# Kernel tuning notes

Hardware: AMD Instinct MI355X
Metric: run time of the kernel (lower is better)

The kernel has to match this reference:

```python
import jax, jax.numpy as jnp
import numpy as np

CHANNELS = 256
REDUCTION = 4
REDUCED = max(1, CHANNELS // REDUCTION)  # 64


def setup_inputs() -> dict:
    key = jax.random.key(0)
    kx, kq, kk, kv, ko = jax.random.split(key, 5)
    B, C, H, W = 4, CHANNELS, 48, 48
    x = jax.random.normal(kx, (B, C, H, W), dtype=jnp.float32)
    # 1x1 conv weights (bias=False) for 3 q/k/v branches, stored as [3, reduced, C]
    wq = jax.random.normal(kq, (3, REDUCED, C), dtype=jnp.float32) * 0.05
    wk = jax.random.normal(kk, (3, REDUCED, C), dtype=jnp.float32) * 0.05
    wv = jax.random.normal(kv, (3, REDUCED, C), dtype=jnp.float32) * 0.05
    # output 1x1 conv: [C, 3*reduced]
    wo = jax.random.normal(ko, (C, 3 * REDUCED), dtype=jnp.float32) * 0.05
    return {"x": x, "wq": wq, "wk": wk, "wv": wv, "wo": wo}


def reference(x, wq, wk, wv, wo):
    B, C, H, W = x.shape
    N = H * W
    r = wq.shape[1]
    scale = 1.0 / float(r) ** 0.5
    xf = x.reshape(B, C, N)                      # [B, C, N]
    # 1x1 convs == channel matmuls; all 3 branches at once
    qs = jnp.einsum('irc,bcn->ibrn', wq, xf)     # [3, B, r, N]
    ks = jnp.einsum('irc,bcn->ibrn', wk, xf)
    vs = jnp.einsum('irc,bcn->ibrn', wv, xf)
    outs = []
    for i in range(3):                           # structural 3x3 nesting
        q = qs[i]                                # [B, r, N]
        acc = jnp.zeros((B, r, N), dtype=x.dtype)
        for j in range(3):
            # attn[b, n, m] = softmax_m(q[b,:,n] . k[b,:,m] / sqrt(r))
            attn = jax.nn.softmax(jnp.einsum('brn,brm->bnm', q, ks[j]) * scale, axis=-1)
            acc = acc + jnp.einsum('brm,bnm->brn', vs[j], attn)
        outs.append(acc)
    combined = jnp.concatenate(outs, axis=1)     # [B, 3r, N]
    out = jnp.einsum('cr,brn->bcn', wo, combined).reshape(B, C, H, W)
    return x * jax.nn.sigmoid(out)
```

## Files before the change

kernel.cpp:

```cpp
#include <hip/hip_runtime.h>


#define BB 4
#define CC 256
#define NN_ 2304
#define RR 64

#define OQ 0
#define OK_ 1769472
#define OV 3538944
#define OC 5308416
#define CSTR 1769472
#define FR_IB 147456
#define OXF 10616832
#define OWF 12976128
#define OWOF 13123584

typedef __bf16 bf16x8 __attribute__((ext_vector_type(8)));
typedef float f32x16 __attribute__((ext_vector_type(16)));
typedef unsigned short ushort8 __attribute__((ext_vector_type(8)));
typedef unsigned int uintx2 __attribute__((ext_vector_type(2)));
typedef unsigned int uintx4 __attribute__((ext_vector_type(4)));

#if __has_builtin(__builtin_amdgcn_exp2f)
#define EXP2(x) __builtin_amdgcn_exp2f(x)
#else
#define EXP2(x) exp2f(x)
#endif

__device__ __forceinline__ float bf2f(unsigned short s) {
    unsigned int u = ((unsigned int)s) << 16;
    return __builtin_bit_cast(float, u);
}
__device__ __forceinline__ unsigned int pk_bf16(float lo, float hi) {
    unsigned int r;
    asm("v_cvt_pk_bf16_f32 %0, %1, %2" : "=v"(r) : "v"(lo), "v"(hi));
    return r;
}

__global__ __launch_bounds__(256) void prep_kernel(
    const float* __restrict__ x, const float* __restrict__ wq,
    const float* __restrict__ wk, const float* __restrict__ wv,
    const float* __restrict__ wo, unsigned short* __restrict__ wsb)
{
    int bid = blockIdx.x;
    int t = threadIdx.x;
    if (bid < 9) {
        int s = bid;
        int type = s / 3, i = s % 3;
        const float* wsel = (type == 0) ? wq : (type == 1 ? wk : wv);
        const float scale = (type == 0) ? 0.18033688011112042f : 1.0f;
        unsigned short* dst = wsb + OWF + s * 16384;
        #pragma unroll
        for (int p = 0; p < 8; ++p) {
            int u = t + 256 * p;
            int ks = u >> 7, rb = (u >> 6) & 1, lo = u & 63;
            int row = rb * 32 + (lo & 31), c = ks * 16 + 8 * (lo >> 5);
            const float* src = wsel + ((i * 64 + row) * 256 + c);
            float4 f0 = *(const float4*)(src);
            float4 f1 = *(const float4*)(src + 4);
            uintx4 pwv = {pk_bf16(f0.x * scale, f0.y * scale),
                          pk_bf16(f0.z * scale, f0.w * scale),
                          pk_bf16(f1.x * scale, f1.y * scale),
                          pk_bf16(f1.z * scale, f1.w * scale)};
            *(uintx4*)(dst + (ks * 2 + rb) * 512 + lo * 8) = pwv;
        }
        return;
    }
    if (bid < 12) {
        int bb = bid - 9;
        #pragma unroll
        for (int p = 0; p < 8; ++p) {
            int u = t + 256 * p;
            int cg = bb * 32 + (u >> 6);
            int lane = u & 63;
            int ks = cg >> 3, rb = cg & 7;
            int row = rb * 32 + (lane & 31);
            int g = ks * 16 + 8 * (lane >> 5);
            const float* src = wo + row * 192 + g;
            float4 f0 = *(const float4*)(src);
            float4 f1 = *(const float4*)(src + 4);
            uintx4 pwv = {pk_bf16(f0.x, f0.y), pk_bf16(f0.z, f0.w),
                          pk_bf16(f1.x, f1.y), pk_bf16(f1.z, f1.w)};
            *(uintx4*)(wsb + OWOF + cg * 512 + lane * 8) = pwv;
        }
        return;
    }
    __shared__ __align__(16) float xs[64 * 132];
    int xb = bid - 12;
    int cq  = xb & 3;
    int nt2 = (xb >> 2) % 18;
    int b   = xb / 72;
    int c0 = cq * 64, n0 = nt2 * 128;
    #pragma unroll
    for (int p = 0; p < 8; ++p) {
        int u = t + 256 * p;
        int cl = u >> 5, nq = (u & 31) * 4;
        *(float4*)&xs[cl * 132 + nq] =
            *(const float4*)&x[((size_t)(b * CC + c0 + cl)) * NN_ + n0 + nq];
    }
    __syncthreads();
    unsigned short* xfb = wsb + OXF + ((size_t)b) * 72 * 16 * 512;
    #pragma unroll
    for (int p = 0; p < 4; ++p) {
        int u = t + 256 * p;
        int nb_l = u >> 8, ks_l = (u >> 6) & 3, lo = u & 63;
        int hh = lo >> 5, idx = lo & 31;
        int clb = ks_l * 16 + 8 * hh;
        int nn = nb_l * 32 + idx;
        unsigned int pw[4];
        #pragma unroll
        for (int d = 0; d < 4; ++d) {
            float a  = xs[(clb + 2 * d) * 132 + nn];
            float bb2 = xs[(clb + 2 * d + 1) * 132 + nn];
            pw[d] = pk_bf16(a, bb2);
        }
        int nb = nt2 * 4 + nb_l, ks = cq * 4 + ks_l;
        *(uintx4*)(xfb + (nb * 16 + ks) * 512 + lo * 8) =
            (uintx4){pw[0], pw[1], pw[2], pw[3]};
    }
}

__global__ __launch_bounds__(256) void proj_mfma(unsigned short* __restrict__ wsb)
{
    int bid = blockIdx.x;
    int s = bid / 72;
    int rem = bid % 72;
    int b = rem / 18, nb4 = rem % 18;
    int type = s / 3, i = s % 3;
    int t = threadIdx.x;
    int w = t >> 6, lane = t & 63;
    int lq = lane & 31, h = lane >> 5;
    int nb = nb4 * 4 + w;

    const unsigned short* wf = wsb + OWF + s * 16384 + lane * 8;
    const unsigned short* xf = wsb + OXF + ((size_t)(b * 72 + nb) * 16) * 512 + lane * 8;

    f32x16 o0 = {}, o1 = {};
    if (type < 2) {
        #pragma unroll
        for (int ks = 0; ks < 16; ++ks) {
            bf16x8 a0 = *(const bf16x8*)(wf + ks * 1024);
            bf16x8 a1 = *(const bf16x8*)(wf + ks * 1024 + 512);
            bf16x8 bx = *(const bf16x8*)(xf + ks * 512);
            o0 = __builtin_amdgcn_mfma_f32_32x32x16_bf16(a0, bx, o0, 0, 0, 0);
            o1 = __builtin_amdgcn_mfma_f32_32x32x16_bf16(a1, bx, o1, 0, 0, 0);
        }
    } else {
        #pragma unroll
        for (int ks = 0; ks < 16; ++ks) {
            bf16x8 a0 = *(const bf16x8*)(wf + ks * 1024);
            bf16x8 a1 = *(const bf16x8*)(wf + ks * 1024 + 512);
            bf16x8 bx = *(const bf16x8*)(xf + ks * 512);
            o0 = __builtin_amdgcn_mfma_f32_32x32x16_bf16(bx, a0, o0, 0, 0, 0);
            o1 = __builtin_amdgcn_mfma_f32_32x32x16_bf16(bx, a1, o1, 0, 0, 0);
        }
    }

    unsigned short* dstbase =
        wsb + ((type == 0) ? OQ : (type == 1 ? OK_ : OV)) +
        ((size_t)(i * 4 + b)) * FR_IB + nb * 2048;

    if (type < 2) {
        #pragma unroll
        for (int g = 0; g < 4; ++g) {
            int kd = 8 * g + 4 * h;
            int off = (kd >> 4) * 512 + ((kd >> 3) & 1) * 256 + lq * 8 + (kd & 7);
            *(uintx2*)(dstbase + off) =
                (uintx2){pk_bf16(o0[4 * g], o0[4 * g + 1]),
                         pk_bf16(o0[4 * g + 2], o0[4 * g + 3])};
            int kd2 = kd + 32;
            int off2 = (kd2 >> 4) * 512 + ((kd2 >> 3) & 1) * 256 + lq * 8 + (kd2 & 7);
            *(uintx2*)(dstbase + off2) =
                (uintx2){pk_bf16(o1[4 * g], o1[4 * g + 1]),
                         pk_bf16(o1[4 * g + 2], o1[4 * g + 3])};
        }
    } else {
        #pragma unroll
        for (int g = 0; g < 4; ++g) {
            int off = (g >> 1) * 1024 + (g & 1) * 256 + lq * 8 + 4 * h;
            *(uintx2*)(dstbase + off) =
                (uintx2){pk_bf16(o0[4 * g], o0[4 * g + 1]),
                         pk_bf16(o0[4 * g + 2], o0[4 * g + 3])};
            *(uintx2*)(dstbase + off + 512) =
                (uintx2){pk_bf16(o1[4 * g], o1[4 * g + 1]),
                         pk_bf16(o1[4 * g + 2], o1[4 * g + 3])};
        }
    }
}

__global__ __launch_bounds__(256, 4) void attn_kernel(unsigned short* __restrict__ wsb)
{
    __shared__ __align__(16) float fl[4352];

    int bid = blockIdx.x;
    int wid = (bid & 7) * 162 + (bid >> 3);
    int s12 = wid / 108;
    int rem = wid % 108;
    int j = s12 >> 2, b = s12 & 3;
    int i = rem / 36;
    int qp = rem % 36;
    int w = threadIdx.x >> 6;
    int ks = w & 1, qloc = w >> 1;
    int lane = threadIdx.x & 63;
    int lq = lane & 31;
    int h = lane >> 5;
    int q0 = (qp * 2 + qloc) * 32;
    int nt = q0 >> 5;

    const unsigned short* qtf = wsb + OQ + ((size_t)(i * 4 + b)) * FR_IB +
                                nt * 2048 + lane * 8;
    const unsigned short* kp = wsb + OK_ + ((size_t)(j * 4 + b)) * FR_IB +
                               (size_t)(ks * 36) * 2048 + lane * 8;
    const unsigned short* vp = wsb + OV + ((size_t)(j * 4 + b)) * FR_IB +
                               (size_t)(ks * 36) * 2048 + lane * 8;

    bf16x8 bq0 = *(const bf16x8*)(qtf + 0);
    bf16x8 bq1 = *(const bf16x8*)(qtf + 512);
    bf16x8 bq2 = *(const bf16x8*)(qtf + 1024);
    bf16x8 bq3 = *(const bf16x8*)(qtf + 1536);

    uintx4 onesw = {0x3F803F80u, 0x3F803F80u, 0x3F803F80u, 0x3F803F80u};
    bf16x8 ones = __builtin_bit_cast(bf16x8, onesw);

    f32x16 o0 = {}, o1 = {}, lacc = {};

    for (int step = 0; step < 36; ++step) {
        const unsigned short* kb = kp + (size_t)step * 2048;
        const unsigned short* vb = vp + (size_t)step * 2048;
        bf16x8 k0 = *(const bf16x8*)(kb + 0 * 512);
        bf16x8 k1 = *(const bf16x8*)(kb + 1 * 512);
        bf16x8 k2 = *(const bf16x8*)(kb + 2 * 512);
        bf16x8 k3 = *(const bf16x8*)(kb + 3 * 512);
        bf16x8 v00 = *(const bf16x8*)(vb + 0 * 512);
        bf16x8 v10 = *(const bf16x8*)(vb + 1 * 512);
        bf16x8 v01 = *(const bf16x8*)(vb + 2 * 512);
        bf16x8 v11 = *(const bf16x8*)(vb + 3 * 512);

        f32x16 s = {};
        __builtin_amdgcn_s_setprio(1);
        s = __builtin_amdgcn_mfma_f32_32x32x16_bf16(k0, bq0, s, 0, 0, 0);
        s = __builtin_amdgcn_mfma_f32_32x32x16_bf16(k1, bq1, s, 0, 0, 0);
        s = __builtin_amdgcn_mfma_f32_32x32x16_bf16(k2, bq2, s, 0, 0, 0);
        s = __builtin_amdgcn_mfma_f32_32x32x16_bf16(k3, bq3, s, 0, 0, 0);
        __builtin_amdgcn_s_setprio(0);

        #pragma unroll
        for (int r = 0; r < 16; ++r) s[r] = EXP2(s[r]);

        __builtin_amdgcn_s_setprio(1);
        {
            unsigned int a0 = pk_bf16(s[0], s[1]);
            unsigned int a1 = pk_bf16(s[2], s[3]);
            unsigned int b0 = pk_bf16(s[4], s[5]);
            unsigned int b1 = pk_bf16(s[6], s[7]);
            uintx2 r0 = __builtin_amdgcn_permlane32_swap(a0, b0, false, false);
            uintx2 r1 = __builtin_amdgcn_permlane32_swap(a1, b1, false, false);
            uintx4 pwv = {r0[0], r1[0], r0[1], r1[1]};
            bf16x8 pa = __builtin_bit_cast(bf16x8, pwv);
            o0 = __builtin_amdgcn_mfma_f32_32x32x16_bf16(v00, pa, o0, 0, 0, 0);
            o1 = __builtin_amdgcn_mfma_f32_32x32x16_bf16(v10, pa, o1, 0, 0, 0);
            lacc = __builtin_amdgcn_mfma_f32_32x32x16_bf16(ones, pa, lacc, 0, 0, 0);
        }
        {
            unsigned int a0 = pk_bf16(s[8], s[9]);
            unsigned int a1 = pk_bf16(s[10], s[11]);
            unsigned int b0 = pk_bf16(s[12], s[13]);
            unsigned int b1 = pk_bf16(s[14], s[15]);
            uintx2 r0 = __builtin_amdgcn_permlane32_swap(a0, b0, false, false);
            uintx2 r1 = __builtin_amdgcn_permlane32_swap(a1, b1, false, false);
            uintx4 pwv = {r0[0], r1[0], r0[1], r1[1]};
            bf16x8 pa = __builtin_bit_cast(bf16x8, pwv);
            o0 = __builtin_amdgcn_mfma_f32_32x32x16_bf16(v01, pa, o0, 0, 0, 0);
            o1 = __builtin_amdgcn_mfma_f32_32x32x16_bf16(v11, pa, o1, 0, 0, 0);
            lacc = __builtin_amdgcn_mfma_f32_32x32x16_bf16(ones, pa, lacc, 0, 0, 0);
        }
        __builtin_amdgcn_s_setprio(0);
    }

    float l_full = lacc[0];

    int off = qloc * 2112;
    if (ks == 1) {
        #pragma unroll
        for (int reg = 0; reg < 16; ++reg) {
            fl[off + reg * 64 + lane] = o0[reg];
            fl[off + 1024 + reg * 64 + lane] = o1[reg];
        }
        fl[off + 2048 + lane] = l_full;
    }
    __syncthreads();
    if (ks == 1) return;

    #pragma unroll
    for (int reg = 0; reg < 16; ++reg) {
        o0[reg] += fl[off + reg * 64 + lane];
        o1[reg] += fl[off + 1024 + reg * 64 + lane];
    }
    float l_tot = l_full + fl[off + 2048 + lane];
    __syncthreads();

    float inv = 1.f / l_tot;
    o0 *= inv; o1 *= inv;

    float* tw = fl + qloc * 2080;
    #pragma unroll
    for (int reg = 0; reg < 16; ++reg) {
        int rv = (reg & 3) + 8 * (reg >> 2) + 4 * h;
        tw[lq * 65 + rv] = o0[reg];
        tw[lq * 65 + 32 + rv] = o1[reg];
    }
    unsigned short* cb = wsb + OC + (size_t)j * CSTR +
                         ((size_t)((b * 72 + nt) * 12 + i * 4)) * 512;
    #pragma unroll
    for (int ksl = 0; ksl < 4; ++ksl) {
        const float* src = tw + lq * 65 + ksl * 16 + 8 * h;
        uintx4 pwv = {pk_bf16(src[0], src[1]), pk_bf16(src[2], src[3]),
                      pk_bf16(src[4], src[5]), pk_bf16(src[6], src[7])};
        *(uintx4*)(cb + ksl * 512 + lane * 8) = pwv;
    }
}

__global__ __launch_bounds__(256) void out_mfma(
    const float* __restrict__ x, const unsigned short* __restrict__ wsb,
    float* __restrict__ out)
{
    int bid = blockIdx.x;
    int ch = bid & 1;
    int nt = (bid >> 1) % 72;
    int b  = bid / 144;
    int n0 = nt * 32;
    int t = threadIdx.x;
    int w = t >> 6, lane = t & 63;
    int lq = lane & 31, h = lane >> 5;
    int rb = ch * 4 + w;

    const unsigned short* wof = wsb + OWOF + lane * 8;
    const unsigned short* cbase = wsb + OC +
        ((size_t)((b * 72 + nt) * 12)) * 512 + lane * 8;

    f32x16 acc = {};
    #pragma unroll
    for (int j = 0; j < 3; ++j) {
        const unsigned short* cj = cbase + (size_t)j * CSTR;
        #pragma unroll
        for (int ksx = 0; ksx < 12; ++ksx) {
            bf16x8 bx = *(const bf16x8*)(cj + ksx * 512);
            bf16x8 a0 = *(const bf16x8*)(wof + (ksx * 8 + rb) * 512);
            acc = __builtin_amdgcn_mfma_f32_32x32x16_bf16(a0, bx, acc, 0, 0, 0);
        }
    }

    int c0 = rb * 32;
    #pragma unroll
    for (int reg = 0; reg < 16; ++reg) {
        int c = c0 + (reg & 3) + 8 * (reg >> 2) + 4 * h;
        size_t idx = ((size_t)(b * CC + c)) * NN_ + n0 + lq;
        float sg = 1.f / (1.f + EXP2(acc[reg] * -1.44269504f));
        out[idx] = x[idx] * sg;
    }
}

extern "C" void kernel_launch(void* const* d_in, const int* in_sizes, int n_in,
                              void* d_out, int out_size, void* d_ws, size_t ws_size,
                              hipStream_t stream) {
    const float* x  = (const float*)d_in[0];
    const float* wq = (const float*)d_in[1];
    const float* wk = (const float*)d_in[2];
    const float* wv = (const float*)d_in[3];
    const float* wo = (const float*)d_in[4];
    unsigned short* wsb = (unsigned short*)d_ws;
    float* out = (float*)d_out;

    prep_kernel<<<300, 256, 0, stream>>>(x, wq, wk, wv, wo, wsb);
    proj_mfma<<<648, 256, 0, stream>>>(wsb);
    attn_kernel<<<1296, 256, 0, stream>>>(wsb);
    out_mfma<<<576, 256, 0, stream>>>(x, wsb, out);
}
```

Before: 102.8 us.

## Prefetch K fragments one step ahead and compute softmax row sums with VALU

The attention inner loop is restructured to double-buffer K fragment loads, issuing the next step's K reads before the current step's MFMAs so global latency overlaps with compute. The per-step ones-vector MFMA used to accumulate the softmax denominator is replaced by scalar float adds of the exponentiated scores, followed by a cross-half-wave shuffle. The s_setprio hints are also removed. These changes cut MFMA work and load stalls, but add register pressure, and the denominator is now summed in fp32 instead of from the bf16-rounded probabilities.

```diff
diff --git a/kernel.cpp b/kernel.cpp
--- a/kernel.cpp
+++ b/kernel.cpp
@@ -220,35 +220,28 @@
     bf16x8 bq2 = *(const bf16x8*)(qtf + 1024);
     bf16x8 bq3 = *(const bf16x8*)(qtf + 1536);
 
-    uintx4 onesw = {0x3F803F80u, 0x3F803F80u, 0x3F803F80u, 0x3F803F80u};
-    bf16x8 ones = __builtin_bit_cast(bf16x8, onesw);
-
-    f32x16 o0 = {}, o1 = {}, lacc = {};
-
-    for (int step = 0; step < 36; ++step) {
-        const unsigned short* kb = kp + (size_t)step * 2048;
+    f32x16 o0 = {}, o1 = {};
+    float l_loc = 0.f;
+
+    auto compute_step = [&](bf16x8 k0, bf16x8 k1, bf16x8 k2, bf16x8 k3,
+                            int step) {
         const unsigned short* vb = vp + (size_t)step * 2048;
-        bf16x8 k0 = *(const bf16x8*)(kb + 0 * 512);
-        bf16x8 k1 = *(const bf16x8*)(kb + 1 * 512);
-        bf16x8 k2 = *(const bf16x8*)(kb + 2 * 512);
-        bf16x8 k3 = *(const bf16x8*)(kb + 3 * 512);
         bf16x8 v00 = *(const bf16x8*)(vb + 0 * 512);
         bf16x8 v10 = *(const bf16x8*)(vb + 1 * 512);
         bf16x8 v01 = *(const bf16x8*)(vb + 2 * 512);
         bf16x8 v11 = *(const bf16x8*)(vb + 3 * 512);
 
         f32x16 s = {};
-        __builtin_amdgcn_s_setprio(1);
         s = __builtin_amdgcn_mfma_f32_32x32x16_bf16(k0, bq0, s, 0, 0, 0);
         s = __builtin_amdgcn_mfma_f32_32x32x16_bf16(k1, bq1, s, 0, 0, 0);
         s = __builtin_amdgcn_mfma_f32_32x32x16_bf16(k2, bq2, s, 0, 0, 0);
         s = __builtin_amdgcn_mfma_f32_32x32x16_bf16(k3, bq3, s, 0, 0, 0);
-        __builtin_amdgcn_s_setprio(0);
 
         #pragma unroll
         for (int r = 0; r < 16; ++r) s[r] = EXP2(s[r]);
-
-        __builtin_amdgcn_s_setprio(1);
+        l_loc += ((s[0] + s[1]) + (s[2] + s[3])) + ((s[4] + s[5]) + (s[6] + s[7])) +
+                 ((s[8] + s[9]) + (s[10] + s[11])) + ((s[12] + s[13]) + (s[14] + s[15]));
+
         {
             unsigned int a0 = pk_bf16(s[0], s[1]);
             unsigned int a1 = pk_bf16(s[2], s[3]);
@@ -260,7 +253,6 @@
             bf16x8 pa = __builtin_bit_cast(bf16x8, pwv);
             o0 = __builtin_amdgcn_mfma_f32_32x32x16_bf16(v00, pa, o0, 0, 0, 0);
             o1 = __builtin_amdgcn_mfma_f32_32x32x16_bf16(v10, pa, o1, 0, 0, 0);
-            lacc = __builtin_amdgcn_mfma_f32_32x32x16_bf16(ones, pa, lacc, 0, 0, 0);
         }
         {
             unsigned int a0 = pk_bf16(s[8], s[9]);
@@ -273,12 +265,34 @@
             bf16x8 pa = __builtin_bit_cast(bf16x8, pwv);
             o0 = __builtin_amdgcn_mfma_f32_32x32x16_bf16(v01, pa, o0, 0, 0, 0);
             o1 = __builtin_amdgcn_mfma_f32_32x32x16_bf16(v11, pa, o1, 0, 0, 0);
-            lacc = __builtin_amdgcn_mfma_f32_32x32x16_bf16(ones, pa, lacc, 0, 0, 0);
-        }
-        __builtin_amdgcn_s_setprio(0);
-    }
-
-    float l_full = lacc[0];
+        }
+    };
+
+    bf16x8 kA0 = *(const bf16x8*)(kp + 0 * 512);
+    bf16x8 kA1 = *(const bf16x8*)(kp + 1 * 512);
+    bf16x8 kA2 = *(const bf16x8*)(kp + 2 * 512);
+    bf16x8 kA3 = *(const bf16x8*)(kp + 3 * 512);
+
+    for (int step = 0; step < 36; step += 2) {
+        const unsigned short* kbB = kp + (size_t)(step + 1) * 2048;
+        bf16x8 kB0 = *(const bf16x8*)(kbB + 0 * 512);
+        bf16x8 kB1 = *(const bf16x8*)(kbB + 1 * 512);
+        bf16x8 kB2 = *(const bf16x8*)(kbB + 2 * 512);
+        bf16x8 kB3 = *(const bf16x8*)(kbB + 3 * 512);
+
+        compute_step(kA0, kA1, kA2, kA3, step);
+
+        int nx = (step + 2 < 36) ? (step + 2) : 0;
+        const unsigned short* kbA = kp + (size_t)nx * 2048;
+        kA0 = *(const bf16x8*)(kbA + 0 * 512);
+        kA1 = *(const bf16x8*)(kbA + 1 * 512);
+        kA2 = *(const bf16x8*)(kbA + 2 * 512);
+        kA3 = *(const bf16x8*)(kbA + 3 * 512);
+
+        compute_step(kB0, kB1, kB2, kB3, step + 1);
+    }
+
+    float l_full = l_loc + __shfl_xor(l_loc, 32);
 
     int off = qloc * 2112;
     if (ks == 1) {
```

New measurement: 96.70 us. 1.06x faster.

## Prefetch next K tile, compute row sums with VALU, drop setprio, raise occupancy

Applied to the files above, without the earlier changes.

The loop now loads the K fragments for the next step right after the QK MFMAs, so the global load latency overlaps with the exp and PV work. The softmax denominator is now summed with VALU adds in fp32 plus a cross-half shuffle, replacing the two extra MFMAs against a ones vector. The s_setprio hints are removed and launch bounds are raised to 5 waves per SIMD. This frees MFMA cycles and hides load latency, at the cost of more VALU work and tighter register limits. The denominator is also now summed from fp32 values rather than bf16-rounded ones.

```diff
diff --git a/kernel.cpp b/kernel.cpp
--- a/kernel.cpp
+++ b/kernel.cpp
@@ -189,7 +189,7 @@
     }
 }
 
-__global__ __launch_bounds__(256, 4) void attn_kernel(unsigned short* __restrict__ wsb)
+__global__ __launch_bounds__(256, 5) void attn_kernel(unsigned short* __restrict__ wsb)
 {
     __shared__ __align__(16) float fl[4352];
 
@@ -220,35 +220,41 @@
     bf16x8 bq2 = *(const bf16x8*)(qtf + 1024);
     bf16x8 bq3 = *(const bf16x8*)(qtf + 1536);
 
-    uintx4 onesw = {0x3F803F80u, 0x3F803F80u, 0x3F803F80u, 0x3F803F80u};
-    bf16x8 ones = __builtin_bit_cast(bf16x8, onesw);
-
-    f32x16 o0 = {}, o1 = {}, lacc = {};
+    f32x16 o0 = {}, o1 = {};
+    float l_loc = 0.f;
+
+    bf16x8 k0 = *(const bf16x8*)(kp + 0 * 512);
+    bf16x8 k1 = *(const bf16x8*)(kp + 1 * 512);
+    bf16x8 k2 = *(const bf16x8*)(kp + 2 * 512);
+    bf16x8 k3 = *(const bf16x8*)(kp + 3 * 512);
 
     for (int step = 0; step < 36; ++step) {
-        const unsigned short* kb = kp + (size_t)step * 2048;
         const unsigned short* vb = vp + (size_t)step * 2048;
-        bf16x8 k0 = *(const bf16x8*)(kb + 0 * 512);
-        bf16x8 k1 = *(const bf16x8*)(kb + 1 * 512);
-        bf16x8 k2 = *(const bf16x8*)(kb + 2 * 512);
-        bf16x8 k3 = *(const bf16x8*)(kb + 3 * 512);
         bf16x8 v00 = *(const bf16x8*)(vb + 0 * 512);
         bf16x8 v10 = *(const bf16x8*)(vb + 1 * 512);
         bf16x8 v01 = *(const bf16x8*)(vb + 2 * 512);
         bf16x8 v11 = *(const bf16x8*)(vb + 3 * 512);
 
         f32x16 s = {};
-        __builtin_amdgcn_s_setprio(1);
         s = __builtin_amdgcn_mfma_f32_32x32x16_bf16(k0, bq0, s, 0, 0, 0);
         s = __builtin_amdgcn_mfma_f32_32x32x16_bf16(k1, bq1, s, 0, 0, 0);
         s = __builtin_amdgcn_mfma_f32_32x32x16_bf16(k2, bq2, s, 0, 0, 0);
         s = __builtin_amdgcn_mfma_f32_32x32x16_bf16(k3, bq3, s, 0, 0, 0);
-        __builtin_amdgcn_s_setprio(0);
+
+        {
+            int nx = (step + 1 < 36) ? (step + 1) : 0;
+            const unsigned short* kb = kp + (size_t)nx * 2048;
+            k0 = *(const bf16x8*)(kb + 0 * 512);
+            k1 = *(const bf16x8*)(kb + 1 * 512);
+            k2 = *(const bf16x8*)(kb + 2 * 512);
+            k3 = *(const bf16x8*)(kb + 3 * 512);
+        }
 
         #pragma unroll
         for (int r = 0; r < 16; ++r) s[r] = EXP2(s[r]);
-
-        __builtin_amdgcn_s_setprio(1);
+        l_loc += ((s[0] + s[1]) + (s[2] + s[3])) + ((s[4] + s[5]) + (s[6] + s[7])) +
+                 ((s[8] + s[9]) + (s[10] + s[11])) + ((s[12] + s[13]) + (s[14] + s[15]));
+
         {
             unsigned int a0 = pk_bf16(s[0], s[1]);
             unsigned int a1 = pk_bf16(s[2], s[3]);
@@ -260,7 +266,6 @@
             bf16x8 pa = __builtin_bit_cast(bf16x8, pwv);
             o0 = __builtin_amdgcn_mfma_f32_32x32x16_bf16(v00, pa, o0, 0, 0, 0);
             o1 = __builtin_amdgcn_mfma_f32_32x32x16_bf16(v10, pa, o1, 0, 0, 0);
-            lacc = __builtin_amdgcn_mfma_f32_32x32x16_bf16(ones, pa, lacc, 0, 0, 0);
         }
         {
             unsigned int a0 = pk_bf16(s[8], s[9]);
@@ -273,12 +278,10 @@
             bf16x8 pa = __builtin_bit_cast(bf16x8, pwv);
             o0 = __builtin_amdgcn_mfma_f32_32x32x16_bf16(v01, pa, o0, 0, 0, 0);
             o1 = __builtin_amdgcn_mfma_f32_32x32x16_bf16(v11, pa, o1, 0, 0, 0);
-            lacc = __builtin_amdgcn_mfma_f32_32x32x16_bf16(ones, pa, lacc, 0, 0, 0);
-        }
-        __builtin_amdgcn_s_setprio(0);
-    }
-
-    float l_full = lacc[0];
+        }
+    }
+
+    float l_full = l_loc + __shfl_xor(l_loc, 32);
 
     int off = qloc * 2112;
     if (ks == 1) {
```

Measured after the change: 98.76 us. -3.9%, faster.
